# Optimization experiments

Hardware: AMD Instinct MI355X
Metric: run time of the kernel (lower is better)

## Reference

```python
import jax, jax.numpy as jnp
import numpy as np

GRID_SIZE = 5
SPLINE_ORDER = 3
GRID_RANGE = (-0.2, 0.2)
N_TOK, IN_CH, OUT_CH = 8192, 1024, 1024
K_COEF = GRID_SIZE + SPLINE_ORDER  # 8 basis functions per feature


def _make_grid():
    lo, hi = GRID_RANGE
    h = (hi - lo) / GRID_SIZE
    # 12 knots, extended by spline_order on both sides
    return (jnp.arange(-SPLINE_ORDER, GRID_SIZE + SPLINE_ORDER + 1, dtype=jnp.float32) * h + lo)


def _b_splines(x, grid):
    # x: [N, in] -> bases: [N, in, K_COEF] via Cox-de Boor recursion
    xe = x[..., None]                      # [N, in, 1]
    G = grid.shape[0]                      # 12
    bases = ((xe >= grid[:-1]) & (xe < grid[1:])).astype(x.dtype)  # [N, in, G-1]
    for k in range(1, SPLINE_ORDER + 1):
        left = (xe - grid[: G - k - 1]) / (grid[k : G - 1] - grid[: G - k - 1]) * bases[..., :-1]
        right = (grid[k + 1 :] - xe) / (grid[k + 1 :] - grid[1 : G - k]) * bases[..., 1:]
        bases = left + right
    return bases                            # [N, in, 8]


def _kan_layer(x, base_w, spline_w, grid):
    # base_activation = Identity
    base_out = x @ base_w.T                               # [N, out]
    bases = _b_splines(x, grid)                           # [N, in, K]
    spline_out = jnp.einsum('nik,oik->no', bases, spline_w)
    return base_out + spline_out


def setup_inputs() -> dict:
    key = jax.random.key(0)
    k1, k2, k3, k4, k5 = jax.random.split(key, 5)
    lo, hi = GRID_RANGE
    x = jax.random.uniform(k1, (N_TOK, IN_CH), dtype=jnp.float32, minval=lo, maxval=hi)
    s = 0.1 / np.sqrt(IN_CH)
    return {
        'x': x,
        'base_w1': jax.random.normal(k2, (OUT_CH, IN_CH), dtype=jnp.float32) * s,
        'spline_w1': jax.random.normal(k3, (OUT_CH, IN_CH, K_COEF), dtype=jnp.float32) * s,
        'base_w2': jax.random.normal(k4, (OUT_CH, OUT_CH), dtype=jnp.float32) * s,
        'spline_w2': jax.random.normal(k5, (OUT_CH, OUT_CH, K_COEF), dtype=jnp.float32) * s,
    }


def reference(x, base_w1, spline_w1, base_w2, spline_w2):
    grid = _make_grid()
    x1 = _kan_layer(x, base_w1, spline_w1, grid)
    x2 = _kan_layer(x1, base_w2, spline_w2, grid)
    return x2
```

## Files before the change

kernel.cpp:

```cpp
#include <hip/hip_runtime.h>
#include <hip/hip_bf16.h>

typedef __attribute__((ext_vector_type(8))) short bf16x8;
typedef __attribute__((ext_vector_type(4))) float f32x4;

#define KCAT 9216
#define NTOK 8192
#define CH   1024
#define KHALF 4608
#define BK   64
#define NT   (KHALF / BK)

__device__ __forceinline__ unsigned short f2bf(float f) {
    union { float f; unsigned int u; } v; v.f = f;
    unsigned int r = v.u + 0x7fffu + ((v.u >> 16) & 1u);
    return (unsigned short)(r >> 16);
}

__device__ __forceinline__ void load16_to_lds(const void* gp, void* lp) {
    __builtin_amdgcn_global_load_lds(
        (__attribute__((address_space(1))) void*)(void*)gp,
        (__attribute__((address_space(3))) void*)lp,
        16, 0, 0);
}

__device__ __forceinline__ void bases8(float x, unsigned short* out8) {
    const float h = 0.08f;
    float t[12];
#pragma unroll
    for (int j = 0; j < 12; ++j) t[j] = -0.2f + h * (float)(j - 3);
    const float r1 = 1.0f / h, r2 = 1.0f / (2.0f * h), r3 = 1.0f / (3.0f * h);
    float b[11];
#pragma unroll
    for (int j = 0; j < 11; ++j) b[j] = (x >= t[j] && x < t[j + 1]) ? 1.0f : 0.0f;
#pragma unroll
    for (int j = 0; j < 10; ++j) b[j] = (x - t[j]) * r1 * b[j] + (t[j + 2] - x) * r1 * b[j + 1];
#pragma unroll
    for (int j = 0; j < 9; ++j)  b[j] = (x - t[j]) * r2 * b[j] + (t[j + 3] - x) * r2 * b[j + 1];
#pragma unroll
    for (int j = 0; j < 8; ++j)  b[j] = (x - t[j]) * r3 * b[j] + (t[j + 4] - x) * r3 * b[j + 1];
#pragma unroll
    for (int j = 0; j < 8; ++j) out8[j] = f2bf(b[j]);
}

__global__ __launch_bounds__(256) void conv_w(const float* __restrict__ BW,
                                              const float* __restrict__ SW,
                                              unsigned short* __restrict__ W) {
    int o = blockIdx.x;
    const float* bw = BW + (size_t)o * 1024;
    const float* sw = SW + (size_t)o * 8192;
    unsigned short* w = W + (size_t)o * KCAT;
    for (int c = threadIdx.x * 4; c < KCAT; c += 256 * 4) {
        const float* src = (c < 1024) ? (bw + c) : (sw + (c - 1024));
        float4 v = *(const float4*)src;
        unsigned short u[4] = { f2bf(v.x), f2bf(v.y), f2bf(v.z), f2bf(v.w) };
        *(unsigned long long*)(w + c) = *(unsigned long long*)u;
    }
}

__global__ __launch_bounds__(256) void kan_basis_x(const float* __restrict__ X,
                                                   unsigned short* __restrict__ A,
                                                   int total) {
    for (int idx = blockIdx.x * 256 + threadIdx.x; idx < total; idx += gridDim.x * 256) {
        int n = idx >> 10, i = idx & 1023;
        float x = X[idx];
        size_t rowbase = (size_t)n * KCAT;
        A[rowbase + i] = f2bf(x);
        unsigned short out8[8];
        bases8(x, out8);
        *(bf16x8*)(A + rowbase + 1024 + (size_t)i * 8) = *(bf16x8*)out8;
    }
}

__global__ __launch_bounds__(256) void kan_basis_sum(const float* __restrict__ C0,
                                                     const float* __restrict__ C1,
                                                     unsigned short* __restrict__ A,
                                                     int total) {
    for (int idx = blockIdx.x * 256 + threadIdx.x; idx < total; idx += gridDim.x * 256) {
        int n = idx >> 10, i = idx & 1023;
        float x = C0[idx] + C1[idx];
        size_t rowbase = (size_t)n * KCAT;
        A[rowbase + i] = f2bf(x);
        unsigned short out8[8];
        bases8(x, out8);
        *(bf16x8*)(A + rowbase + 1024 + (size_t)i * 8) = *(bf16x8*)out8;
    }
}

__global__ __launch_bounds__(256) void add_out(const float* __restrict__ C0,
                                               const float* __restrict__ C1,
                                               float* __restrict__ out, int total4) {
    for (int i = blockIdx.x * 256 + threadIdx.x; i < total4; i += gridDim.x * 256) {
        float4 a = ((const float4*)C0)[i];
        float4 b = ((const float4*)C1)[i];
        float4 r = { a.x + b.x, a.y + b.y, a.z + b.z, a.w + b.w };
        ((float4*)out)[i] = r;
    }
}

__global__ __launch_bounds__(512, 2) void gemm256_splitk(const unsigned short* __restrict__ A,
                                                         const unsigned short* __restrict__ B,
                                                         float* __restrict__ C0,
                                                         float* __restrict__ C1) {
    __shared__ unsigned short As[2 * 256 * 64];
    __shared__ unsigned short Bs[2 * 256 * 64];
    const int tid  = threadIdx.x;
    const int lane = tid & 63;
    const int wid  = tid >> 6;
    const int wr = wid >> 2, wc = wid & 3;
    const int ln = lane & 15, q = lane >> 4;

    const int bid = blockIdx.x;
    const int xcd = bid & 7, i = bid >> 3;
    const int kz = xcd & 1, chm = xcd >> 1;
    const int bm = chm * 8 + (i & 7);
    const int bn = i >> 3;

    const unsigned short* Ab = A + (size_t)(bm * 256) * KCAT + (size_t)kz * KHALF;
    const unsigned short* Bb = B + (size_t)(bn * 256) * KCAT + (size_t)kz * KHALF;
    float* C = (kz == 0) ? C0 : C1;

    f32x4 acc[8][4] = {};

    auto stage = [&](int t, int buf, int part) {
        int chunk = part * 512 + tid;
        int r    = chunk >> 3;
        int slot = (chunk & 7) ^ (r & 7);
        size_t goff = (size_t)r * (KCAT * 2) + (size_t)t * (BK * 2) + slot * 16;
        load16_to_lds((const char*)Ab + goff, (char*)As + (size_t)buf * 32768 + chunk * 16);
        load16_to_lds((const char*)Bb + goff, (char*)Bs + (size_t)buf * 32768 + chunk * 16);
    };

    stage(0, 0, 0); stage(0, 0, 1); stage(0, 0, 2); stage(0, 0, 3);
    asm volatile("s_waitcnt vmcnt(0)" ::: "memory");
    __builtin_amdgcn_s_barrier();

    for (int t = 0; t < NT; ++t) {
        const int c = t & 1;
        const char* Ap = (const char*)As + c * 32768;
        const char* Bp = (const char*)Bs + c * 32768;
        bf16x8 bfr[4][2];
        const bool pref = (t + 1 < NT);
#pragma unroll
        for (int p = 0; p < 4; ++p) {
            bf16x8 afr[2][2];
#pragma unroll
            for (int m2 = 0; m2 < 2; ++m2)
#pragma unroll
                for (int kh = 0; kh < 2; ++kh) {
                    int row = wr * 128 + (p * 2 + m2) * 16 + ln;
                    int byte = row * 128 + ((kh * 64 + q * 16) ^ ((row & 7) * 16));
                    afr[m2][kh] = *(const bf16x8*)(Ap + byte);
                }
            if (p == 0) {
#pragma unroll
                for (int nf = 0; nf < 4; ++nf)
#pragma unroll
                    for (int kh = 0; kh < 2; ++kh) {
                        int row = wc * 64 + nf * 16 + ln;
                        int byte = row * 128 + ((kh * 64 + q * 16) ^ ((row & 7) * 16));
                        bfr[nf][kh] = *(const bf16x8*)(Bp + byte);
                    }
            }
            if (pref) {
                if (p == 0)      { stage(t + 1, c ^ 1, 0); stage(t + 1, c ^ 1, 1); }
                else if (p == 1) { stage(t + 1, c ^ 1, 2); }
                else if (p == 2) { stage(t + 1, c ^ 1, 3); }
            }
            __builtin_amdgcn_s_barrier();
            asm volatile("s_waitcnt lgkmcnt(0)" ::: "memory");
            __builtin_amdgcn_sched_barrier(0);
            __builtin_amdgcn_s_setprio(1);
#pragma unroll
            for (int m2 = 0; m2 < 2; ++m2)
#pragma unroll
                for (int nf = 0; nf < 4; ++nf)
#pragma unroll
                    for (int kh = 0; kh < 2; ++kh)
                        acc[p * 2 + m2][nf] = __builtin_amdgcn_mfma_f32_16x16x32_bf16(
                            afr[m2][kh], bfr[nf][kh], acc[p * 2 + m2][nf], 0, 0, 0);
            __builtin_amdgcn_s_setprio(0);
            if (p == 3)
                asm volatile("s_waitcnt vmcnt(0)" ::: "memory");
            __builtin_amdgcn_s_barrier();
        }
    }

#pragma unroll
    for (int mf = 0; mf < 8; ++mf)
#pragma unroll
        for (int nf = 0; nf < 4; ++nf)
#pragma unroll
            for (int r = 0; r < 4; ++r) {
                int row = bm * 256 + wr * 128 + mf * 16 + q * 4 + r;
                int col = bn * 256 + wc * 64 + nf * 16 + ln;
                C[(size_t)row * CH + col] = acc[mf][nf][r];
            }
}

extern "C" void kernel_launch(void* const* d_in, const int* in_sizes, int n_in,
                              void* d_out, int out_size, void* d_ws, size_t ws_size,
                              hipStream_t stream) {
    const float* x   = (const float*)d_in[0];
    const float* bw1 = (const float*)d_in[1];
    const float* sw1 = (const float*)d_in[2];
    const float* bw2 = (const float*)d_in[3];
    const float* sw2 = (const float*)d_in[4];
    float* out = (float*)d_out;

    char* ws = (char*)d_ws;
    unsigned short* Abuf = (unsigned short*)ws;
    unsigned short* Wbuf = (unsigned short*)(ws + 150994944);
    float* C0 = (float*)(ws + 150994944 + 18874368);
    float* C1 = (float*)(ws + 150994944 + 18874368 + 33554432);

    dim3 blk(256);
    dim3 gW(1024);
    dim3 gB(2048);
    dim3 gG(256);
    dim3 blkG(512);

    conv_w        <<<gW, blk, 0, stream>>>(bw1, sw1, Wbuf);
    kan_basis_x   <<<gB, blk, 0, stream>>>(x, Abuf, NTOK * CH);
    gemm256_splitk<<<gG, blkG, 0, stream>>>(Abuf, Wbuf, C0, C1);

    conv_w        <<<gW, blk, 0, stream>>>(bw2, sw2, Wbuf);
    kan_basis_sum <<<gB, blk, 0, stream>>>(C0, C1, Abuf, NTOK * CH);
    gemm256_splitk<<<gG, blkG, 0, stream>>>(Abuf, Wbuf, C0, C1);
    add_out       <<<dim3(1024), blk, 0, stream>>>(C0, C1, out, NTOK * CH / 4);
}
```

Before: 506.7 us.

## Use closed-form cubic B-spline bases, fuse prep kernels, and deepen GEMM LDS pipeline

New measurement: 544.8 us. +7.5%, slower.

```diff
diff --git a/kernel.cpp b/kernel.cpp
--- a/kernel.cpp
+++ b/kernel.cpp
@@ -3,6 +3,7 @@
 
 typedef __attribute__((ext_vector_type(8))) short bf16x8;
 typedef __attribute__((ext_vector_type(4))) float f32x4;
+typedef __attribute__((ext_vector_type(4))) unsigned int u32x4;
 
 #define KCAT 9216
 #define NTOK 8192
@@ -10,6 +11,7 @@
 #define KHALF 4608
 #define BK   64
 #define NT   (KHALF / BK)
+#define NH   (2 * NT)
 
 __device__ __forceinline__ unsigned short f2bf(float f) {
     union { float f; unsigned int u; } v; v.f = f;
@@ -24,29 +26,38 @@
         16, 0, 0);
 }
 
-__device__ __forceinline__ void bases8(float x, unsigned short* out8) {
-    const float h = 0.08f;
-    float t[12];
-#pragma unroll
-    for (int j = 0; j < 12; ++j) t[j] = -0.2f + h * (float)(j - 3);
-    const float r1 = 1.0f / h, r2 = 1.0f / (2.0f * h), r3 = 1.0f / (3.0f * h);
-    float b[11];
-#pragma unroll
-    for (int j = 0; j < 11; ++j) b[j] = (x >= t[j] && x < t[j + 1]) ? 1.0f : 0.0f;
-#pragma unroll
-    for (int j = 0; j < 10; ++j) b[j] = (x - t[j]) * r1 * b[j] + (t[j + 2] - x) * r1 * b[j + 1];
-#pragma unroll
-    for (int j = 0; j < 9; ++j)  b[j] = (x - t[j]) * r2 * b[j] + (t[j + 3] - x) * r2 * b[j + 1];
-#pragma unroll
-    for (int j = 0; j < 8; ++j)  b[j] = (x - t[j]) * r3 * b[j] + (t[j + 4] - x) * r3 * b[j + 1];
-#pragma unroll
-    for (int j = 0; j < 8; ++j) out8[j] = f2bf(b[j]);
-}
-
-__global__ __launch_bounds__(256) void conv_w(const float* __restrict__ BW,
-                                              const float* __restrict__ SW,
-                                              unsigned short* __restrict__ W) {
-    int o = blockIdx.x;
+__device__ __forceinline__ void bases8_cf(float x, unsigned int* w) {
+    float p  = (x + 0.44f) * 12.5f;
+    float mf = floorf(p);
+    float u  = p - mf;
+    int   m  = (int)mf;
+    float v  = 1.0f - u;
+    float u2 = u * u, u3 = u2 * u;
+    float N0 = v * v * v * (1.0f / 6.0f);
+    float N1 = 0.5f * u3 - u2 + (2.0f / 3.0f);
+    float N3 = u3 * (1.0f / 6.0f);
+    float N2 = 1.0f - N0 - N1 - N3;
+    unsigned long long lo =
+          (unsigned long long)f2bf(N0)
+        | ((unsigned long long)f2bf(N1) << 16)
+        | ((unsigned long long)f2bf(N2) << 32)
+        | ((unsigned long long)f2bf(N3) << 48);
+    lo = (m >= 0 && m <= 10) ? lo : 0ull;
+    int sh  = (m - 3) * 16;
+    int sh1 = sh - 64;
+    unsigned long long d0 =
+        (sh  >= 0) ? ((sh  < 64) ? (lo << sh)    : 0ull)
+                   : ((-sh  < 64) ? (lo >> (-sh))  : 0ull);
+    unsigned long long d1 =
+        (sh1 >= 0) ? ((sh1 < 64) ? (lo << sh1)   : 0ull)
+                   : ((-sh1 < 64) ? (lo >> (-sh1)) : 0ull);
+    w[0] = (unsigned int)d0; w[1] = (unsigned int)(d0 >> 32);
+    w[2] = (unsigned int)d1; w[3] = (unsigned int)(d1 >> 32);
+}
+
+__device__ __forceinline__ void conv_w_body(const float* __restrict__ BW,
+                                            const float* __restrict__ SW,
+                                            unsigned short* __restrict__ W, int o) {
     const float* bw = BW + (size_t)o * 1024;
     const float* sw = SW + (size_t)o * 8192;
     unsigned short* w = W + (size_t)o * KCAT;
@@ -58,33 +69,38 @@
     }
 }
 
-__global__ __launch_bounds__(256) void kan_basis_x(const float* __restrict__ X,
-                                                   unsigned short* __restrict__ A,
-                                                   int total) {
-    for (int idx = blockIdx.x * 256 + threadIdx.x; idx < total; idx += gridDim.x * 256) {
-        int n = idx >> 10, i = idx & 1023;
-        float x = X[idx];
-        size_t rowbase = (size_t)n * KCAT;
-        A[rowbase + i] = f2bf(x);
-        unsigned short out8[8];
-        bases8(x, out8);
-        *(bf16x8*)(A + rowbase + 1024 + (size_t)i * 8) = *(bf16x8*)out8;
-    }
-}
-
-__global__ __launch_bounds__(256) void kan_basis_sum(const float* __restrict__ C0,
-                                                     const float* __restrict__ C1,
-                                                     unsigned short* __restrict__ A,
-                                                     int total) {
-    for (int idx = blockIdx.x * 256 + threadIdx.x; idx < total; idx += gridDim.x * 256) {
-        int n = idx >> 10, i = idx & 1023;
-        float x = C0[idx] + C1[idx];
-        size_t rowbase = (size_t)n * KCAT;
-        A[rowbase + i] = f2bf(x);
-        unsigned short out8[8];
-        bases8(x, out8);
-        *(bf16x8*)(A + rowbase + 1024 + (size_t)i * 8) = *(bf16x8*)out8;
-    }
+__device__ __forceinline__ void basis_body(float x, unsigned short* __restrict__ A, int idx) {
+    int n = idx >> 10, i = idx & 1023;
+    size_t rowbase = (size_t)n * KCAT;
+    A[rowbase + i] = f2bf(x);
+    unsigned int w[4];
+    bases8_cf(x, w);
+    *(u32x4*)(A + rowbase + 1024 + (size_t)i * 8) = (u32x4){w[0], w[1], w[2], w[3]};
+}
+
+__global__ __launch_bounds__(256) void prep1(const float* __restrict__ BW1,
+                                             const float* __restrict__ SW1,
+                                             unsigned short* __restrict__ W,
+                                             const float* __restrict__ X,
+                                             unsigned short* __restrict__ A) {
+    int b = blockIdx.x;
+    if (b < 1024) { conv_w_body(BW1, SW1, W, b); return; }
+    int bb = b - 1024;
+    for (int idx = bb * 256 + threadIdx.x; idx < NTOK * CH; idx += 2048 * 256)
+        basis_body(X[idx], A, idx);
+}
+
+__global__ __launch_bounds__(256) void mid2(const float* __restrict__ BW2,
+                                            const float* __restrict__ SW2,
+                                            unsigned short* __restrict__ W,
+                                            const float* __restrict__ C0,
+                                            const float* __restrict__ C1,
+                                            unsigned short* __restrict__ A) {
+    int b = blockIdx.x;
+    if (b < 1024) { conv_w_body(BW2, SW2, W, b); return; }
+    int bb = b - 1024;
+    for (int idx = bb * 256 + threadIdx.x; idx < NTOK * CH; idx += 2048 * 256)
+        basis_body(C0[idx] + C1[idx], A, idx);
 }
 
 __global__ __launch_bounds__(256) void add_out(const float* __restrict__ C0,
@@ -102,8 +118,8 @@
                                                          const unsigned short* __restrict__ B,
                                                          float* __restrict__ C0,
                                                          float* __restrict__ C1) {
-    __shared__ unsigned short As[2 * 256 * 64];
-    __shared__ unsigned short Bs[2 * 256 * 64];
+    __shared__ __align__(16) unsigned short As[4 * 256 * 32];
+    __shared__ __align__(16) unsigned short Bs[4 * 256 * 32];
     const int tid  = threadIdx.x;
     const int lane = tid & 63;
     const int wid  = tid >> 6;
@@ -111,10 +127,10 @@
     const int ln = lane & 15, q = lane >> 4;
 
     const int bid = blockIdx.x;
-    const int xcd = bid & 7, i = bid >> 3;
+    const int xcd = bid & 7, ii = bid >> 3;
     const int kz = xcd & 1, chm = xcd >> 1;
-    const int bm = chm * 8 + (i & 7);
-    const int bn = i >> 3;
+    const int bm = chm * 8 + (ii & 7);
+    const int bn = ii >> 3;
 
     const unsigned short* Ab = A + (size_t)(bm * 256) * KCAT + (size_t)kz * KHALF;
     const unsigned short* Bb = B + (size_t)(bn * 256) * KCAT + (size_t)kz * KHALF;
@@ -122,67 +138,76 @@
 
     f32x4 acc[8][4] = {};
 
-    auto stage = [&](int t, int buf, int part) {
-        int chunk = part * 512 + tid;
-        int r    = chunk >> 3;
-        int slot = (chunk & 7) ^ (r & 7);
-        size_t goff = (size_t)r * (KCAT * 2) + (size_t)t * (BK * 2) + slot * 16;
-        load16_to_lds((const char*)Ab + goff, (char*)As + (size_t)buf * 32768 + chunk * 16);
-        load16_to_lds((const char*)Bb + goff, (char*)Bs + (size_t)buf * 32768 + chunk * 16);
+    auto stageA2 = [&](int ts, int ks, int ds) {
+#pragma unroll
+        for (int part = 0; part < 2; ++part) {
+            int c = part * 512 + tid;
+            int r = c >> 2;
+            int gslot = (c & 3) ^ ((r >> 1) & 3);
+            size_t goff = (size_t)r * (KCAT * 2) + (size_t)ts * 128 + ks * 64 + gslot * 16;
+            load16_to_lds((const char*)Ab + goff, (char*)As + (size_t)ds * 16384 + c * 16);
+        }
     };
-
-    stage(0, 0, 0); stage(0, 0, 1); stage(0, 0, 2); stage(0, 0, 3);
-    asm volatile("s_waitcnt vmcnt(0)" ::: "memory");
+    auto stageB2 = [&](int ts, int ks, int ds) {
+#pragma unroll
+        for (int part = 0; part < 2; ++part) {
+            int c = part * 512 + tid;
+            int r = c >> 2;
+            int gslot = (c & 3) ^ ((r >> 1) & 3);
+            size_t goff = (size_t)r * (KCAT * 2) + (size_t)ts * 128 + ks * 64 + gslot * 16;
+            load16_to_lds((const char*)Bb + goff, (char*)Bs + (size_t)ds * 16384 + c * 16);
+        }
+    };
+
+    stageA2(0, 0, 0); stageB2(0, 0, 0);
+    stageA2(0, 1, 1); stageB2(0, 1, 1);
+    asm volatile("s_waitcnt vmcnt(4)" ::: "memory");
     __builtin_amdgcn_s_barrier();
 
     for (int t = 0; t < NT; ++t) {
-        const int c = t & 1;
-        const char* Ap = (const char*)As + c * 32768;
-        const char* Bp = (const char*)Bs + c * 32768;
-        bf16x8 bfr[4][2];
-        const bool pref = (t + 1 < NT);
-#pragma unroll
-        for (int p = 0; p < 4; ++p) {
-            bf16x8 afr[2][2];
-#pragma unroll
-            for (int m2 = 0; m2 < 2; ++m2)
-#pragma unroll
-                for (int kh = 0; kh < 2; ++kh) {
-                    int row = wr * 128 + (p * 2 + m2) * 16 + ln;
-                    int byte = row * 128 + ((kh * 64 + q * 16) ^ ((row & 7) * 16));
-                    afr[m2][kh] = *(const bf16x8*)(Ap + byte);
+#pragma unroll
+        for (int kh = 0; kh < 2; ++kh) {
+            const int j  = 2 * t + kh;
+            const int sl = j & 3;
+            const char* Ah = (const char*)As + sl * 16384;
+            const char* Bh = (const char*)Bs + sl * 16384;
+            const int jn = j + 2;
+            const bool pf = jn < NH;
+            const int ts = jn >> 1, ks = jn & 1, ds = jn & 3;
+            bf16x8 bfr[4];
+#pragma unroll
+            for (int ph = 0; ph < 2; ++ph) {
+                bf16x8 afr[4];
+#pragma unroll
+                for (int m = 0; m < 4; ++m) {
+                    int row = wr * 128 + (ph * 4 + m) * 16 + ln;
+                    afr[m] = *(const bf16x8*)(Ah + row * 64 + ((q ^ ((row >> 1) & 3)) * 16));
                 }
-            if (p == 0) {
-#pragma unroll
-                for (int nf = 0; nf < 4; ++nf)
-#pragma unroll
-                    for (int kh = 0; kh < 2; ++kh) {
+                if (ph == 0) {
+#pragma unroll
+                    for (int nf = 0; nf < 4; ++nf) {
                         int row = wc * 64 + nf * 16 + ln;
-                        int byte = row * 128 + ((kh * 64 + q * 16) ^ ((row & 7) * 16));
-                        bfr[nf][kh] = *(const bf16x8*)(Bp + byte);
+                        bfr[nf] = *(const bf16x8*)(Bh + row * 64 + ((q ^ ((row >> 1) & 3)) * 16));
                     }
+                }
+                if (pf) { if (ph == 0) stageA2(ts, ks, ds); else stageB2(ts, ks, ds); }
+                __builtin_amdgcn_s_barrier();
+                asm volatile("s_waitcnt lgkmcnt(0)" ::: "memory");
+                __builtin_amdgcn_sched_barrier(0);
+                __builtin_amdgcn_s_setprio(1);
+#pragma unroll
+                for (int m = 0; m < 4; ++m)
+#pragma unroll
+                    for (int nf = 0; nf < 4; ++nf)
+                        acc[ph * 4 + m][nf] = __builtin_amdgcn_mfma_f32_16x16x32_bf16(
+                            afr[m], bfr[nf], acc[ph * 4 + m][nf], 0, 0, 0);
+                __builtin_amdgcn_s_setprio(0);
+                if (ph == 1) {
+                    if (pf)               asm volatile("s_waitcnt vmcnt(4)" ::: "memory");
+                    else if (j + 1 < NH)  asm volatile("s_waitcnt vmcnt(0)" ::: "memory");
+                }
+                __builtin_amdgcn_s_barrier();
             }
-            if (pref) {
-                if (p == 0)      { stage(t + 1, c ^ 1, 0); stage(t + 1, c ^ 1, 1); }
-                else if (p == 1) { stage(t + 1, c ^ 1, 2); }
-                else if (p == 2) { stage(t + 1, c ^ 1, 3); }
-            }
-            __builtin_amdgcn_s_barrier();
-            asm volatile("s_waitcnt lgkmcnt(0)" ::: "memory");
-            __builtin_amdgcn_sched_barrier(0);
-            __builtin_amdgcn_s_setprio(1);
-#pragma unroll
-            for (int m2 = 0; m2 < 2; ++m2)
-#pragma unroll
-                for (int nf = 0; nf < 4; ++nf)
-#pragma unroll
-                    for (int kh = 0; kh < 2; ++kh)
-                        acc[p * 2 + m2][nf] = __builtin_amdgcn_mfma_f32_16x16x32_bf16(
-                            afr[m2][kh], bfr[nf][kh], acc[p * 2 + m2][nf], 0, 0, 0);
-            __builtin_amdgcn_s_setprio(0);
-            if (p == 3)
-                asm volatile("s_waitcnt vmcnt(0)" ::: "memory");
-            __builtin_amdgcn_s_barrier();
         }
     }
 
@@ -214,18 +239,10 @@
     float* C0 = (float*)(ws + 150994944 + 18874368);
     float* C1 = (float*)(ws + 150994944 + 18874368 + 33554432);
 
-    dim3 blk(256);
-    dim3 gW(1024);
-    dim3 gB(2048);
-    dim3 gG(256);
-    dim3 blkG(512);
-
-    conv_w        <<<gW, blk, 0, stream>>>(bw1, sw1, Wbuf);
-    kan_basis_x   <<<gB, blk, 0, stream>>>(x, Abuf, NTOK * CH);
-    gemm256_splitk<<<gG, blkG, 0, stream>>>(Abuf, Wbuf, C0, C1);
-
-    conv_w        <<<gW, blk, 0, stream>>>(bw2, sw2, Wbuf);
-    kan_basis_sum <<<gB, blk, 0, stream>>>(C0, C1, Abuf, NTOK * CH);
-    gemm256_splitk<<<gG, blkG, 0, stream>>>(Abuf, Wbuf, C0, C1);
-    add_out       <<<dim3(1024), blk, 0, stream>>>(C0, C1, out, NTOK * CH / 4);
-}
+    prep1         <<<dim3(3072), dim3(256), 0, stream>>>(bw1, sw1, Wbuf, x, Abuf);
+    gemm256_splitk<<<dim3(256), dim3(512), 0, stream>>>(Abuf, Wbuf, C0, C1);
+
+    mid2          <<<dim3(3072), dim3(256), 0, stream>>>(bw2, sw2, Wbuf, C0, C1, Abuf);
+    gemm256_splitk<<<dim3(256), dim3(512), 0, stream>>>(Abuf, Wbuf, C0, C1);
+    add_out       <<<dim3(1024), dim3(256), 0, stream>>>(C0, C1, out, NTOK * CH / 4);
+}
```
